# Optimization experiments

Measured on AMD Instinct MI355X. Metric: run time of the kernel, lower is better.

Reference implementation:

```python
import jax, jax.numpy as jnp
import numpy as np

BETA = 1.0
EPS_MU = 1e-6
EPS_LOG = 1e-8
D_DIM = 2048
M_EVENTS = 16384
T_HORIZON = 100


def setup_inputs() -> dict:
    key = jax.random.key(0)
    k1, k2 = jax.random.split(key)
    # sorted event times in [0, T_HORIZON)
    t_events = jnp.sort(jax.random.uniform(k1, (M_EVENTS,), jnp.float32) * T_HORIZON)
    marks = jax.random.randint(k2, (M_EVENTS,), 0, D_DIM)  # int marks in {0..D-1}
    # learned params, init exactly as in torch module
    log_mu = jnp.full((D_DIM,), -3.0, jnp.float32)
    log_alpha = jnp.full((D_DIM, D_DIM), -4.0, jnp.float32)
    return {
        "t_events": t_events,
        "marks": marks,
        "T_max": T_HORIZON,
        "log_mu": log_mu,
        "log_alpha": log_alpha,
    }


def _loglik(t_events, log_mu, log_alpha, marks, T_max, beta=BETA):
    mu = jax.nn.softplus(log_mu) + EPS_MU          # [D]
    alpha = jax.nn.softplus(log_alpha)             # [D, D]
    D = mu.shape[0]
    # dt[0] = 0 so the first step leaves S (= zeros) untouched, matching the
    # torch loop which skips decay at n == 0.
    dt = jnp.concatenate([jnp.zeros((1,), t_events.dtype), jnp.diff(t_events)])  # [M]

    def step(S, xs):
        dt_n, d = xs
        S = jnp.exp(-beta * dt_n) * S              # exponential decay of state [D]
        lam_d = mu[d] + alpha[d] @ S               # intensity at event's mark
        S = S.at[d].add(1.0)                       # self-excitation bump
        return S, jnp.log(lam_d + EPS_LOG)

    _, log_lams = jax.lax.scan(step, jnp.zeros((D,), mu.dtype), (dt, marks))

    # compensator integral term
    T = jnp.asarray(T_max, t_events.dtype)
    one_minus_exp = 1.0 - jnp.exp(-beta * (T - t_events))          # [M]
    contrib = jax.ops.segment_sum(one_minus_exp, marks, num_segments=D)  # [D]
    integral = mu * T + alpha @ (contrib / beta)                   # [D]
    return log_lams.sum() - integral.sum()


def reference(t_events, marks, T_max, log_mu, log_alpha):
    return _loglik(t_events, log_mu, log_alpha, marks, T_max)
```

## Files before the change

kernel.cpp:

```cpp
#include <hip/hip_runtime.h>
#include <math.h>

#define D_DIM 2048
#define M_EV  16384
#define LCH   32
#define CCH   (M_EV / LCH)
#define SEG   32
#define NSEG  (CCH / SEG)
#define BETA  1.0f

__device__ __forceinline__ float softplus_f(float x){
  float e = __expf(-fabsf(x));
  return fmaxf(x, 0.0f) + __logf(1.0f + e);
}

__device__ __forceinline__ float decode_T(const void* p){
  unsigned bits = *(const unsigned*)p;
  float fv = __uint_as_float(bits);
  return (fv >= 1e-3f && fv <= 1e7f) ? fv : (float)(int)bits;
}

__device__ __forceinline__ float wave_red(float v){
  #pragma unroll
  for (int o = 32; o > 0; o >>= 1) v += __shfl_down(v, o);
  return v;
}

__global__ void k_small(const float* __restrict__ t, const int* __restrict__ m,
                        const void* Tp, const float* __restrict__ log_mu,
                        float* __restrict__ muw, float* __restrict__ contrib,
                        float* __restrict__ SL, float* __restrict__ dchunk,
                        float* __restrict__ cumdec, float* __restrict__ Aseg,
                        float* __restrict__ acc){
  const int b = blockIdx.x, tid = threadIdx.x;
  if (b < 8){
    int j = b*256 + tid;
    float v = softplus_f(log_mu[j]) + 1e-6f;
    muw[j] = v;
    float s = wave_red(v);
    if ((tid & 63) == 0) atomicAdd(&acc[2], s);
  } else if (b < 72){
    int i = (b-8)*256 + tid;
    float T = decode_T(Tp);
    float v = 1.0f - __expf(-BETA * (T - t[i]));
    atomicAdd(&contrib[m[i]], v);
  } else if (b < 136){
    int i = (b-72)*256 + tid;
    int c = i >> 5;
    if (c < CCH - 1){
      float tn = t[(c+1)*LCH];
      float v = __expf(-BETA * (tn - t[i]));
      atomicAdd(&SL[(size_t)c * D_DIM + m[i]], v);
    }
  } else {
    int c = (b-136)*256 + tid;
    float tc = t[c*LCH];
    dchunk[c] = (c < CCH-1) ? __expf(-BETA * (t[(c+1)*LCH] - tc)) : 1.0f;
    int s0c = (c >> 5) << 5;
    cumdec[c] = __expf(-BETA * (tc - t[s0c*LCH]));
    if (b == 136 && tid < NSEG){
      int s = tid;
      Aseg[s] = (s < NSEG-1)
        ? __expf(-BETA * (t[(s+1)*SEG*LCH] - t[s*SEG*LCH])) : 1.0f;
    }
  }
}

__global__ void k_scan_local(float* __restrict__ SL,
                             const float* __restrict__ dchunk,
                             float* __restrict__ Carry){
  const int tid = threadIdx.x;
  const int seg = blockIdx.x >> 3, jb = blockIdx.x & 7;
  const int j = jb*256 + tid;
  const int c0 = seg * SEG;
  const size_t base = (size_t)c0 * D_DIM + j;
  float u = 0.f;
  float cur[4], nxt[4];
  #pragma unroll
  for (int q = 0; q < 4; ++q) cur[q] = SL[base + (size_t)q * D_DIM];
  for (int g = 0; g < SEG; g += 4){
    #pragma unroll
    for (int q = 0; q < 4; ++q)
      nxt[q] = (g+4 < SEG) ? SL[base + (size_t)(g+4+q) * D_DIM] : 0.f;
    #pragma unroll
    for (int q = 0; q < 4; ++q){
      int c = c0 + g + q;
      float l = cur[q];
      SL[(size_t)c * D_DIM + j] = u;
      u = fmaf(dchunk[c], u, l);
    }
    #pragma unroll
    for (int q = 0; q < 4; ++q) cur[q] = nxt[q];
  }
  Carry[(size_t)seg * D_DIM + j] = u;
}

__global__ void k_scan_carry(const float* __restrict__ Carry,
                             const float* __restrict__ Aseg,
                             float* __restrict__ E){
  const int j = blockIdx.x*256 + threadIdx.x;
  float cr[NSEG];
  #pragma unroll
  for (int s = 0; s < NSEG; ++s) cr[s] = Carry[(size_t)s * D_DIM + j];
  float e = 0.f;
  #pragma unroll
  for (int s = 0; s < NSEG; ++s){
    E[(size_t)s * D_DIM + j] = e;
    e = fmaf(Aseg[s], e, cr[s]);
  }
}

__global__ __launch_bounds__(256) void k_events(
    const float* __restrict__ t, const int* __restrict__ m,
    const float* __restrict__ la, const float* __restrict__ muw,
    const float* __restrict__ SL, const float* __restrict__ E,
    const float* __restrict__ cumdec, float* __restrict__ acc){
  __shared__ float tl[LCH];
  __shared__ int   ml[LCH];
  __shared__ float red[LCH][4];
  const int tid = threadIdx.x;
  const int c = blockIdx.x;
  const int seg = c >> 5;
  const float cd = cumdec[c];

  const float4* sp = (const float4*)(SL + (size_t)c  * D_DIM + tid*8);
  const float4* ep = (const float4*)(E  + (size_t)seg * D_DIM + tid*8);
  float4 s0 = sp[0], s1 = sp[1];
  float4 e0 = ep[0], e1 = ep[1];
  s0.x = fmaf(e0.x, cd, s0.x); s0.y = fmaf(e0.y, cd, s0.y);
  s0.z = fmaf(e0.z, cd, s0.z); s0.w = fmaf(e0.w, cd, s0.w);
  s1.x = fmaf(e1.x, cd, s1.x); s1.y = fmaf(e1.y, cd, s1.y);
  s1.z = fmaf(e1.z, cd, s1.z); s1.w = fmaf(e1.w, cd, s1.w);

  if (tid < LCH){ tl[tid] = t[c*LCH + tid]; ml[tid] = m[c*LCH + tid]; }
  __syncthreads();

  const int lane = tid & 63, wid = tid >> 6;
  const int colb = tid * 8;

  const float* A0 = la + (size_t)ml[0] * D_DIM + colb;
  float4 a0 = *(const float4*)A0, a1 = *(const float4*)(A0 + 4);

  #pragma unroll 1
  for (int k = 0; k < LCH; ++k){
    const int d = ml[k];
    const int kn = (k < LCH-1) ? k+1 : k;
    const float* Bp = la + (size_t)ml[kn] * D_DIM + colb;
    float4 b0 = *(const float4*)Bp, b1 = *(const float4*)(Bp + 4);

    const float dec = (k == 0) ? 1.0f : __expf(-BETA * (tl[k] - tl[k-1]));
    s0.x *= dec; s0.y *= dec; s0.z *= dec; s0.w *= dec;
    s1.x *= dec; s1.y *= dec; s1.z *= dec; s1.w *= dec;

    float p = 0.f;
    p = fmaf(softplus_f(a0.x), s0.x, p);
    p = fmaf(softplus_f(a0.y), s0.y, p);
    p = fmaf(softplus_f(a0.z), s0.z, p);
    p = fmaf(softplus_f(a0.w), s0.w, p);
    p = fmaf(softplus_f(a1.x), s1.x, p);
    p = fmaf(softplus_f(a1.y), s1.y, p);
    p = fmaf(softplus_f(a1.z), s1.z, p);
    p = fmaf(softplus_f(a1.w), s1.w, p);

    if ((d >> 3) == tid){
      int r = d & 7;
      s0.x += (r==0) ? 1.f : 0.f; s0.y += (r==1) ? 1.f : 0.f;
      s0.z += (r==2) ? 1.f : 0.f; s0.w += (r==3) ? 1.f : 0.f;
      s1.x += (r==4) ? 1.f : 0.f; s1.y += (r==5) ? 1.f : 0.f;
      s1.z += (r==6) ? 1.f : 0.f; s1.w += (r==7) ? 1.f : 0.f;
    }

    float w = wave_red(p);
    if (lane == 0) red[k][wid] = w;

    a0 = b0; a1 = b1;
  }

  __syncthreads();
  float lg = 0.f;
  if (tid < LCH){
    float lam = muw[ml[tid]] + red[tid][0] + red[tid][1]
                             + red[tid][2] + red[tid][3];
    lg = __logf(lam + 1e-8f);
  }
  if (tid < 64){
    float w = wave_red(lg);
    if (tid == 0) atomicAdd(&acc[0], w);
  }
}

__global__ void k_int_alpha(const float* __restrict__ la,
                            const float* __restrict__ contrib,
                            float* __restrict__ acc){
  const int nthreads = gridDim.x * blockDim.x;
  int tid = blockIdx.x * blockDim.x + threadIdx.x;
  const float4* la4 = (const float4*)la;
  float p = 0.f;
  #pragma unroll
  for (int u = 0; u < 8; ++u){
    int i4 = tid + u * nthreads;
    float4 x = la4[i4];
    int col = (i4 * 4) & (D_DIM - 1);
    p = fmaf(softplus_f(x.x), contrib[col+0], p);
    p = fmaf(softplus_f(x.y), contrib[col+1], p);
    p = fmaf(softplus_f(x.z), contrib[col+2], p);
    p = fmaf(softplus_f(x.w), contrib[col+3], p);
  }
  __shared__ float red[4];
  float w = wave_red(p);
  int lane = threadIdx.x & 63, wid = threadIdx.x >> 6;
  if (lane == 0) red[wid] = w;
  __syncthreads();
  if (threadIdx.x == 0) atomicAdd(&acc[1], red[0]+red[1]+red[2]+red[3]);
}

__global__ void k_final(const float* __restrict__ acc, const void* Tp,
                        float* __restrict__ out){
  float T = decode_T(Tp);
  out[0] = acc[0] - (T * acc[2] + acc[1] * (1.0f / BETA));
}

extern "C" void kernel_launch(void* const* d_in, const int* in_sizes, int n_in,
                              void* d_out, int out_size, void* d_ws, size_t ws_size,
                              hipStream_t stream) {
  const float* t_events  = (const float*)d_in[0];
  const int*   marks     = (const int*)  d_in[1];
  const void*  Tp        =               d_in[2];
  const float* log_mu    = (const float*)d_in[3];
  const float* log_alpha = (const float*)d_in[4];
  float* out = (float*)d_out;

  float* ws      = (float*)d_ws;
  float* SL      = ws;
  float* contrib = SL + (size_t)CCH * D_DIM;
  float* acc     = contrib + D_DIM;
  float* Carry   = acc + 16;
  float* E       = Carry + (size_t)NSEG * D_DIM;
  float* muw     = E + (size_t)NSEG * D_DIM;
  float* dchunk  = muw + D_DIM;
  float* cumdec  = dchunk + CCH;
  float* Aseg    = cumdec + CCH;

  size_t zero_floats = (size_t)CCH * D_DIM + D_DIM + 16;
  hipMemsetAsync(d_ws, 0, zero_floats * sizeof(float), stream);

  k_small     <<<138, 256, 0, stream>>>(t_events, marks, Tp, log_mu, muw,
                                        contrib, SL, dchunk, cumdec, Aseg, acc);
  k_scan_local<<<NSEG*8, 256, 0, stream>>>(SL, dchunk, Carry);
  k_scan_carry<<<8, 256, 0, stream>>>(Carry, Aseg, E);
  k_events    <<<CCH, 256, 0, stream>>>(t_events, marks, log_alpha, muw,
                                        SL, E, cumdec, acc);
  k_int_alpha <<<512, 256, 0, stream>>>(log_alpha, contrib, acc);
  k_final     <<<1, 1, 0, stream>>>(acc, Tp, out);
}
```

Baseline: 126.8 us.

## Precompute softplus(alpha) once and deepen row prefetch in event kernel

The alpha-integral kernel now also writes softplus(log_alpha) into a workspace buffer and runs before the event kernel. The event kernel then reads these precomputed values instead of evaluating softplus eight times per row per event. The row prefetch is also deepened from one to two rows ahead. This removes repeated transcendental work in the hot loop, at the cost of a 16 MB write plus reads of that buffer and extra registers for the deeper prefetch.

```diff
diff --git a/kernel.cpp b/kernel.cpp
--- a/kernel.cpp
+++ b/kernel.cpp
@@ -110,9 +110,39 @@
   }
 }
 
+__global__ void k_alpha(const float* __restrict__ la,
+                        const float* __restrict__ contrib,
+                        float* __restrict__ sA, float* __restrict__ acc){
+  const int nthreads = gridDim.x * blockDim.x;
+  int tid = blockIdx.x * blockDim.x + threadIdx.x;
+  const float4* la4 = (const float4*)la;
+  float4* sA4 = (float4*)sA;
+  float p = 0.f;
+  #pragma unroll
+  for (int u = 0; u < 8; ++u){
+    int i4 = tid + u * nthreads;
+    float4 x = la4[i4];
+    float4 sp;
+    sp.x = softplus_f(x.x); sp.y = softplus_f(x.y);
+    sp.z = softplus_f(x.z); sp.w = softplus_f(x.w);
+    sA4[i4] = sp;
+    int col = (i4 * 4) & (D_DIM - 1);
+    p = fmaf(sp.x, contrib[col+0], p);
+    p = fmaf(sp.y, contrib[col+1], p);
+    p = fmaf(sp.z, contrib[col+2], p);
+    p = fmaf(sp.w, contrib[col+3], p);
+  }
+  __shared__ float red[4];
+  float w = wave_red(p);
+  int lane = threadIdx.x & 63, wid = threadIdx.x >> 6;
+  if (lane == 0) red[wid] = w;
+  __syncthreads();
+  if (threadIdx.x == 0) atomicAdd(&acc[1], red[0]+red[1]+red[2]+red[3]);
+}
+
 __global__ __launch_bounds__(256) void k_events(
     const float* __restrict__ t, const int* __restrict__ m,
-    const float* __restrict__ la, const float* __restrict__ muw,
+    const float* __restrict__ sA, const float* __restrict__ muw,
     const float* __restrict__ SL, const float* __restrict__ E,
     const float* __restrict__ cumdec, float* __restrict__ acc){
   __shared__ float tl[LCH];
@@ -138,29 +168,27 @@
   const int lane = tid & 63, wid = tid >> 6;
   const int colb = tid * 8;
 
-  const float* A0 = la + (size_t)ml[0] * D_DIM + colb;
-  float4 a0 = *(const float4*)A0, a1 = *(const float4*)(A0 + 4);
+  const float* P0 = sA + (size_t)ml[0] * D_DIM + colb;
+  float4 a0 = *(const float4*)P0, a1 = *(const float4*)(P0 + 4);
+  const float* P1 = sA + (size_t)ml[1] * D_DIM + colb;
+  float4 b0 = *(const float4*)P1, b1 = *(const float4*)(P1 + 4);
 
   #pragma unroll 1
   for (int k = 0; k < LCH; ++k){
     const int d = ml[k];
-    const int kn = (k < LCH-1) ? k+1 : k;
-    const float* Bp = la + (size_t)ml[kn] * D_DIM + colb;
-    float4 b0 = *(const float4*)Bp, b1 = *(const float4*)(Bp + 4);
+    const int kn = (k + 2 < LCH) ? k + 2 : LCH - 1;
+    const float* Pn = sA + (size_t)ml[kn] * D_DIM + colb;
+    float4 c0v = *(const float4*)Pn, c1v = *(const float4*)(Pn + 4);
 
     const float dec = (k == 0) ? 1.0f : __expf(-BETA * (tl[k] - tl[k-1]));
     s0.x *= dec; s0.y *= dec; s0.z *= dec; s0.w *= dec;
     s1.x *= dec; s1.y *= dec; s1.z *= dec; s1.w *= dec;
 
     float p = 0.f;
-    p = fmaf(softplus_f(a0.x), s0.x, p);
-    p = fmaf(softplus_f(a0.y), s0.y, p);
-    p = fmaf(softplus_f(a0.z), s0.z, p);
-    p = fmaf(softplus_f(a0.w), s0.w, p);
-    p = fmaf(softplus_f(a1.x), s1.x, p);
-    p = fmaf(softplus_f(a1.y), s1.y, p);
-    p = fmaf(softplus_f(a1.z), s1.z, p);
-    p = fmaf(softplus_f(a1.w), s1.w, p);
+    p = fmaf(a0.x, s0.x, p); p = fmaf(a0.y, s0.y, p);
+    p = fmaf(a0.z, s0.z, p); p = fmaf(a0.w, s0.w, p);
+    p = fmaf(a1.x, s1.x, p); p = fmaf(a1.y, s1.y, p);
+    p = fmaf(a1.z, s1.z, p); p = fmaf(a1.w, s1.w, p);
 
     if ((d >> 3) == tid){
       int r = d & 7;
@@ -173,7 +201,7 @@
     float w = wave_red(p);
     if (lane == 0) red[k][wid] = w;
 
-    a0 = b0; a1 = b1;
+    a0 = b0; a1 = b1; b0 = c0v; b1 = c1v;
   }
 
   __syncthreads();
@@ -187,31 +215,6 @@
     float w = wave_red(lg);
     if (tid == 0) atomicAdd(&acc[0], w);
   }
-}
-
-__global__ void k_int_alpha(const float* __restrict__ la,
-                            const float* __restrict__ contrib,
-                            float* __restrict__ acc){
-  const int nthreads = gridDim.x * blockDim.x;
-  int tid = blockIdx.x * blockDim.x + threadIdx.x;
-  const float4* la4 = (const float4*)la;
-  float p = 0.f;
-  #pragma unroll
-  for (int u = 0; u < 8; ++u){
-    int i4 = tid + u * nthreads;
-    float4 x = la4[i4];
-    int col = (i4 * 4) & (D_DIM - 1);
-    p = fmaf(softplus_f(x.x), contrib[col+0], p);
-    p = fmaf(softplus_f(x.y), contrib[col+1], p);
-    p = fmaf(softplus_f(x.z), contrib[col+2], p);
-    p = fmaf(softplus_f(x.w), contrib[col+3], p);
-  }
-  __shared__ float red[4];
-  float w = wave_red(p);
-  int lane = threadIdx.x & 63, wid = threadIdx.x >> 6;
-  if (lane == 0) red[wid] = w;
-  __syncthreads();
-  if (threadIdx.x == 0) atomicAdd(&acc[1], red[0]+red[1]+red[2]+red[3]);
 }
 
 __global__ void k_final(const float* __restrict__ acc, const void* Tp,
@@ -240,6 +243,7 @@
   float* dchunk  = muw + D_DIM;
   float* cumdec  = dchunk + CCH;
   float* Aseg    = cumdec + CCH;
+  float* sA      = Aseg + NSEG;
 
   size_t zero_floats = (size_t)CCH * D_DIM + D_DIM + 16;
   hipMemsetAsync(d_ws, 0, zero_floats * sizeof(float), stream);
@@ -248,8 +252,8 @@
                                         contrib, SL, dchunk, cumdec, Aseg, acc);
   k_scan_local<<<NSEG*8, 256, 0, stream>>>(SL, dchunk, Carry);
   k_scan_carry<<<8, 256, 0, stream>>>(Carry, Aseg, E);
-  k_events    <<<CCH, 256, 0, stream>>>(t_events, marks, log_alpha, muw,
+  k_alpha     <<<512, 256, 0, stream>>>(log_alpha, contrib, sA, acc);
+  k_events    <<<CCH, 256, 0, stream>>>(t_events, marks, sA, muw,
                                         SL, E, cumdec, acc);
-  k_int_alpha <<<512, 256, 0, stream>>>(log_alpha, contrib, acc);
   k_final     <<<1, 1, 0, stream>>>(acc, Tp, out);
 }
```

Result: faster. 120.1 us (-5.3%).
